# Kernel optimization log

Measured on AMD Instinct MI355X. Metric: run time of the kernel, lower is better.

Reference implementation:

```python
import jax, jax.numpy as jnp
import numpy as np
import math

V, B, C, H, W = 4, 8, 512, 16, 16
NH = 8


def setup_inputs() -> dict:
    key = jax.random.key(0)
    ks = jax.random.split(key, 10)
    def n(k, shape, s=1.0):
        return jax.random.normal(k, shape, dtype=jnp.float32) * s
    return dict(
        i=n(ks[0], (V, B, C, H, W)),
        c=n(ks[1], (V, B, C, H, W)),
        j=n(ks[2], (V, B, C, H, W)),
        ln1_g=jnp.ones((C,), jnp.float32), ln1_b=jnp.zeros((C,), jnp.float32),
        ln2_g=jnp.ones((C,), jnp.float32), ln2_b=jnp.zeros((C,), jnp.float32),
        Wq=n(ks[3], (C, C), 0.02), bq=jnp.zeros((C,), jnp.float32),
        Wkv=n(ks[4], (C, 2 * C), 0.02), bkv=jnp.zeros((2 * C,), jnp.float32),
        Wo=n(ks[5], (C, C), 0.02), bo=jnp.zeros((C,), jnp.float32),
        Wfc=n(ks[6], (C, 4 * C), 0.02), bfc=jnp.zeros((4 * C,), jnp.float32),
        Wpr=n(ks[7], (4 * C, C), 0.02), bpr=jnp.zeros((C,), jnp.float32),
    )


def _ln(x, g, b, eps=1e-5):
    mu = jnp.mean(x, axis=-1, keepdims=True)
    var = jnp.mean((x - mu) ** 2, axis=-1, keepdims=True)
    return (x - mu) * jax.lax.rsqrt(var + eps) * g + b


def _gelu_new(x):
    # 0.5*x*(1+tanh(sqrt(2/pi)*(x+0.044715*x^3)))
    k = math.sqrt(2.0 / math.pi)
    return 0.5 * x * (1.0 + jnp.tanh(k * (x + 0.044715 * x ** 3)))


def reference(i, c, j, ln1_g, ln1_b, ln2_g, ln2_b, Wq, bq, Wkv, bkv, Wo, bo, Wfc, bfc, Wpr, bpr):
    v, b, ch, h, w = i.shape
    T = v * h * w
    hd = ch // NH

    def to_seq(x):  # v b c h w -> b (v h w) c
        return jnp.transpose(x, (1, 0, 3, 4, 2)).reshape(b, T, ch)

    # LayerNorm (over channel dim) applied before attention
    qs = _ln(to_seq(i), ln1_g, ln1_b)   # [b, T, c]
    kvs = _ln(to_seq(j), ln1_g, ln1_b)  # [b, T, c]

    q = qs @ Wq + bq                    # [b, T, c]
    kv = kvs @ Wkv + bkv                # [b, T, 2c]
    k, vv = jnp.split(kv, 2, axis=-1)

    def heads(x):  # [b, T, c] -> [b, nh, T, hd]
        return x.reshape(b, T, NH, hd).transpose(0, 2, 1, 3)
    q, k, vv = heads(q), heads(k), heads(vv)

    # block-causal mask: token in view-block r attends to view-blocks <= r
    blk = jnp.arange(T) // (h * w)
    mask = blk[:, None] >= blk[None, :]  # [T, T] bool

    att = jnp.einsum('bhqd,bhkd->bhqk', q, k) * (1.0 / math.sqrt(hd))
    att = jnp.where(mask, att, -jnp.inf)
    att = jax.nn.softmax(att, axis=-1)
    y = jnp.einsum('bhqk,bhkd->bhqd', att, vv)
    y = y.transpose(0, 2, 1, 3).reshape(b, T, ch)
    y = y @ Wo + bo                     # attention output, seq layout

    # residual: ln1(c) + attn
    cs = _ln(to_seq(c), ln1_g, ln1_b) + y
    # MLP with residual
    hcs = _ln(cs, ln2_g, ln2_b)
    cs = cs + (_gelu_new(hcs @ Wfc + bfc) @ Wpr + bpr)

    # b (v h w) c -> v b c h w
    out = cs.reshape(b, v, h, w, ch).transpose(1, 0, 4, 2, 3)
    return out
```

## Files before the change

### kernel.cpp

```cpp
#include <hip/hip_runtime.h>
#include <hip/hip_bf16.h>
#include <math.h>


typedef __bf16 bf16;
typedef __bf16 bf16x8 __attribute__((ext_vector_type(8)));
typedef __bf16 bf16x4 __attribute__((ext_vector_type(4)));
typedef float  f32x4  __attribute__((ext_vector_type(4)));

__device__ __forceinline__ void gload_lds16(const void* g, void* l) {
  __builtin_amdgcn_global_load_lds(
      (__attribute__((address_space(1))) void*)(g),
      (__attribute__((address_space(3))) void*)(l), 16, 0, 0);
}

__global__ __launch_bounds__(256)
void prep_k(const float* __restrict__ Wq, const float* __restrict__ Wkv,
            const float* __restrict__ Wo, const float* __restrict__ Wfc,
            const float* __restrict__ Wpr,
            bf16* __restrict__ WqT, bf16* __restrict__ WkvT,
            bf16* __restrict__ WoT, bf16* __restrict__ WfcT,
            bf16* __restrict__ WprT,
            const float* __restrict__ xi, const float* __restrict__ xj,
            const float* __restrict__ xc,
            const float* __restrict__ g, const float* __restrict__ bb,
            bf16* __restrict__ qs, bf16* __restrict__ kvs,
            bf16* __restrict__ csb)
{
  __shared__ float tt[32][33];
  __shared__ float red[4][32];
  const int t = blockIdx.x;
  const int tid = threadIdx.x;
  if (t < 3072) {
    const float* W; bf16* Wt; int K, N, lognx, tl;
    if (t < 256)       { W = Wq;  Wt = WqT;  K = 512;  N = 512;  lognx = 4; tl = t; }
    else if (t < 768)  { W = Wkv; Wt = WkvT; K = 512;  N = 1024; lognx = 5; tl = t - 256; }
    else if (t < 1024) { W = Wo;  Wt = WoT;  K = 512;  N = 512;  lognx = 4; tl = t - 768; }
    else if (t < 2048) { W = Wfc; Wt = WfcT; K = 512;  N = 2048; lognx = 6; tl = t - 1024; }
    else               { W = Wpr; Wt = WprT; K = 2048; N = 512;  lognx = 4; tl = t - 2048; }
    const int bx = tl & ((1 << lognx) - 1), by = tl >> lognx;
    const int x = tid & 31, y = tid >> 5;
    const int n0 = bx << 5, k0 = by << 5;
#pragma unroll
    for (int yy = y; yy < 32; yy += 8)
      tt[yy][x] = W[(size_t)(k0 + yy) * N + n0 + x];
    __syncthreads();
#pragma unroll
    for (int yy = y; yy < 32; yy += 8)
      Wt[(size_t)(n0 + yy) * K + k0 + x] = (bf16)tt[x][yy];
    return;
  }
  const int u = t - 3072;
  const int sel = u >> 9, bid = u & 511;
  const int hh = bid & 15, b = (bid >> 4) & 7, v = bid >> 7;
  const float* src = (sel == 0) ? xi : ((sel == 1) ? xj : xc);
  const size_t base = ((size_t)(v * 8 + b) * 512) * 256 + (size_t)hh * 16;
  const int q = tid & 3, chb = tid >> 2;
  const int wid = tid >> 6, lane = tid & 63;
  const int cb = chb << 3;

  float gr[8], br[8];
  *(f32x4*)&gr[0] = *(const f32x4*)&g[cb];
  *(f32x4*)&gr[4] = *(const f32x4*)&g[cb + 4];
  *(f32x4*)&br[0] = *(const f32x4*)&bb[cb];
  *(f32x4*)&br[4] = *(const f32x4*)&bb[cb + 4];

  f32x4 x[8];
#pragma unroll
  for (int k = 0; k < 8; ++k)
    x[k] = *(const f32x4*)&src[base + (size_t)(cb + k) * 256 + (q << 2)];

  float s[4] = {0.f, 0.f, 0.f, 0.f}, ss[4] = {0.f, 0.f, 0.f, 0.f};
#pragma unroll
  for (int k = 0; k < 8; ++k)
#pragma unroll
    for (int i = 0; i < 4; ++i) {
      s[i] += x[k][i];
      ss[i] += x[k][i] * x[k][i];
    }
#pragma unroll
  for (int off = 4; off < 64; off <<= 1)
#pragma unroll
    for (int i = 0; i < 4; ++i) {
      s[i] += __shfl_xor(s[i], off);
      ss[i] += __shfl_xor(ss[i], off);
    }
  if (lane < 16) {
    red[wid][(lane & 3) * 4 + (lane >> 2)]      = s[lane >> 2];
    red[wid][16 + (lane & 3) * 4 + (lane >> 2)] = ss[lane >> 2];
  }
  __syncthreads();
  float mu[4], rs[4];
#pragma unroll
  for (int i = 0; i < 4; ++i) {
    const int e = q * 4 + i;
    float st  = red[0][e] + red[1][e] + red[2][e] + red[3][e];
    float sst = red[0][16 + e] + red[1][16 + e] + red[2][16 + e] + red[3][16 + e];
    mu[i] = st * (1.f / 512.f);
    rs[i] = rsqrtf(sst * (1.f / 512.f) - mu[i] * mu[i] + 1e-5f);
  }
  const int tkb = v * 256 + hh * 16 + (q << 2);
  bf16* dstb = (sel == 0) ? qs : ((sel == 1) ? kvs : csb);
#pragma unroll
  for (int i = 0; i < 4; ++i) {
    const size_t orow = ((size_t)b * 1024 + tkb + i) * 512;
    bf16x8 o;
#pragma unroll
    for (int k = 0; k < 8; ++k)
      o[k] = (bf16)((x[k][i] - mu[i]) * rs[i] * gr[k] + br[k]);
    *(bf16x8*)&dstb[orow + cb] = o;
  }
}

__global__ __launch_bounds__(256)
void ln2_k(const bf16* __restrict__ cs, const float* __restrict__ g,
           const float* __restrict__ bb, bf16* __restrict__ hcs)
{
  const int tid = threadIdx.x, wid = tid >> 6, lane = tid & 63;
  const int row = blockIdx.x * 4 + wid;
  const bf16x8 v8 = *(const bf16x8*)&cs[(size_t)row * 512 + lane * 8];
  float v[8];
#pragma unroll
  for (int k = 0; k < 8; ++k) v[k] = (float)v8[k];
  float s = 0.f, ss = 0.f;
#pragma unroll
  for (int k = 0; k < 8; ++k) { s += v[k]; ss += v[k] * v[k]; }
#pragma unroll
  for (int off = 1; off < 64; off <<= 1) {
    s += __shfl_xor(s, off);
    ss += __shfl_xor(ss, off);
  }
  const float mu = s * (1.f / 512.f);
  const float rstd = rsqrtf(ss * (1.f / 512.f) - mu * mu + 1e-5f);
  bf16x8 o;
#pragma unroll
  for (int k = 0; k < 8; ++k) {
    int ch = lane * 8 + k;
    o[k] = (bf16)((v[k] - mu) * rstd * g[ch] + bb[ch]);
  }
  *(bf16x8*)&hcs[(size_t)row * 512 + lane * 8] = o;
}

__global__ __launch_bounds__(256)
void gemm_fc_k(const bf16* __restrict__ A, const bf16* __restrict__ Bt,
               const float* __restrict__ bias, bf16* __restrict__ fo)
{
  const int K = 512;
  __shared__ __align__(16) char smem[34816];
  bf16* As = (bf16*)smem;
  bf16* Bs = (bf16*)(smem + 16384);
  const int tid = threadIdx.x;
  const int wid = tid >> 6, lane = tid & 63;
  const int wr = wid >> 1, wc = wid & 1;
  const int ml = lane & 15, kg = (lane >> 4) << 3;
  const int m0 = blockIdx.x * 128, n0 = blockIdx.y * 128;

  const int e0 = wid * 512 + lane * 8;
  const int r0 = e0 >> 5, c0 = e0 & 31;
  const int e1 = e0 + 2048;
  const int r1 = e1 >> 5, c1 = e1 & 31;

  const bf16* Ag = A + (size_t)m0 * K;
  const bf16* Bg = Bt + (size_t)n0 * K;

  f32x4 acc[4][4] = {};

  gload_lds16(Ag + (size_t)r0 * K + c0, As + wid * 512);
  gload_lds16(Ag + (size_t)r1 * K + c1, As + 2048 + wid * 512);
  gload_lds16(Bg + (size_t)r0 * K + c0, Bs + wid * 512);
  gload_lds16(Bg + (size_t)r1 * K + c1, Bs + 2048 + wid * 512);

  int cur = 0;
  for (int k0 = 0; k0 < K; k0 += 32) {
    __syncthreads();
    if (k0 + 32 < K) {
      const int nb = cur ^ 1, kn = k0 + 32;
      gload_lds16(Ag + (size_t)r0 * K + kn + c0, As + nb * 4096 + wid * 512);
      gload_lds16(Ag + (size_t)r1 * K + kn + c1, As + nb * 4096 + 2048 + wid * 512);
      gload_lds16(Bg + (size_t)r0 * K + kn + c0, Bs + nb * 4096 + wid * 512);
      gload_lds16(Bg + (size_t)r1 * K + kn + c1, Bs + nb * 4096 + 2048 + wid * 512);
    }
    bf16x8 af[4], bfr[4];
#pragma unroll
    for (int mf = 0; mf < 4; ++mf)
      af[mf] = *(const bf16x8*)&As[cur * 4096 + (wr * 64 + mf * 16 + ml) * 32 + kg];
#pragma unroll
    for (int nf = 0; nf < 4; ++nf)
      bfr[nf] = *(const bf16x8*)&Bs[cur * 4096 + (wc * 64 + nf * 16 + ml) * 32 + kg];
#pragma unroll
    for (int mf = 0; mf < 4; ++mf)
#pragma unroll
      for (int nf = 0; nf < 4; ++nf)
        acc[mf][nf] = __builtin_amdgcn_mfma_f32_16x16x32_bf16(
            af[mf], bfr[nf], acc[mf][nf], 0, 0, 0);
    cur ^= 1;
  }

  __syncthreads();
  bf16* OT = (bf16*)smem;
  const int jrow0 = (lane >> 4) << 2;
#pragma unroll
  for (int nf = 0; nf < 4; ++nf) {
    const float bv = bias[n0 + wc * 64 + nf * 16 + ml];
#pragma unroll
    for (int mf = 0; mf < 4; ++mf)
#pragma unroll
      for (int j = 0; j < 4; ++j) {
        float x = acc[mf][nf][j] + bv;
        float u = 0.7978845608f * (x + 0.044715f * x * x * x);
        float e = __expf(2.f * u);
        float th = 1.f - 2.f / (e + 1.f);
        OT[(wr * 64 + mf * 16 + jrow0 + j) * 132 + wc * 64 + nf * 16 + ml] =
            (bf16)(0.5f * x * (1.f + th));
      }
  }
  __syncthreads();
#pragma unroll
  for (int it = 0; it < 8; ++it) {
    const int idx = it * 256 + tid;
    const int cg = idx & 15, r = idx >> 4;
    *(bf16x8*)&fo[(size_t)(m0 + r) * 2048 + n0 + cg * 8] =
        *(const bf16x8*)&OT[r * 132 + cg * 8];
  }
}

enum { EPI_O = 2, EPI_PR = 4 };

template <int EPI>
__global__ __launch_bounds__(512)
void gemmsk_k(const bf16* __restrict__ A, const bf16* __restrict__ Bt,
              const float* __restrict__ bias, const bf16* res,
              void* out0, int K)
{
  __shared__ __align__(16) char smem[49152];
  bf16*  AS = (bf16*)smem;
  bf16*  BS = (bf16*)(smem + 16384);
  float* CF = (float*)smem;

  const int tid = threadIdx.x;
  const int wid = tid >> 6, lane = tid & 63;
  const int half = wid >> 2, w2 = wid & 3;
  const int wr = w2 >> 1, wc = w2 & 1;
  const int ml = lane & 15, kg = (lane >> 4) << 3;
  const int m0 = blockIdx.x * 64, n0 = blockIdx.y * 128;
  const int Kh = K >> 1;

  const int eA = w2 * 512 + lane * 8;
  const int rA = eA >> 5, cA = eA & 31;
  const int eB0 = (w2 * 2) * 512 + lane * 8;
  const int rB0 = eB0 >> 5, cB0 = eB0 & 31;
  const int eB1 = eB0 + 512;
  const int rB1 = eB1 >> 5, cB1 = eB1 & 31;

  const bf16* Ag = A + (size_t)m0 * K + half * Kh;
  const bf16* Bg = Bt + (size_t)n0 * K + half * Kh;

  f32x4 acc[2][4] = {};

  gload_lds16(Ag + (size_t)rA * K + cA, AS + half * 2048 + w2 * 512);
  gload_lds16(Bg + (size_t)rB0 * K + cB0, BS + half * 4096 + (w2 * 2) * 512);
  gload_lds16(Bg + (size_t)rB1 * K + cB1, BS + half * 4096 + (w2 * 2 + 1) * 512);

  int cur = 0;
  for (int k0 = 0; k0 < Kh; k0 += 32) {
    __syncthreads();
    if (k0 + 32 < Kh) {
      const int kn = k0 + 32, nb = cur ^ 1;
      gload_lds16(Ag + (size_t)rA * K + kn + cA,
                  AS + nb * 4096 + half * 2048 + w2 * 512);
      gload_lds16(Bg + (size_t)rB0 * K + kn + cB0,
                  BS + nb * 8192 + half * 4096 + (w2 * 2) * 512);
      gload_lds16(Bg + (size_t)rB1 * K + kn + cB1,
                  BS + nb * 8192 + half * 4096 + (w2 * 2 + 1) * 512);
    }
    const bf16* Ac = AS + cur * 4096 + half * 2048;
    const bf16* Bc = BS + cur * 8192 + half * 4096;
    bf16x8 af[2], bfr[4];
#pragma unroll
    for (int mf = 0; mf < 2; ++mf)
      af[mf] = *(const bf16x8*)&Ac[(wr * 32 + mf * 16 + ml) * 32 + kg];
#pragma unroll
    for (int nf = 0; nf < 4; ++nf)
      bfr[nf] = *(const bf16x8*)&Bc[(wc * 64 + nf * 16 + ml) * 32 + kg];
#pragma unroll
    for (int mf = 0; mf < 2; ++mf)
#pragma unroll
      for (int nf = 0; nf < 4; ++nf)
        acc[mf][nf] = __builtin_amdgcn_mfma_f32_16x16x32_bf16(
            af[mf], bfr[nf], acc[mf][nf], 0, 0, 0);
    cur ^= 1;
  }

  const int jrow0 = (lane >> 4) << 2;
  __syncthreads();
  if (half == 0) {
#pragma unroll
    for (int mf = 0; mf < 2; ++mf)
#pragma unroll
      for (int nf = 0; nf < 4; ++nf)
#pragma unroll
        for (int j = 0; j < 4; ++j)
          CF[(wr * 32 + mf * 16 + jrow0 + j) * 128 + wc * 64 + nf * 16 + ml] =
              acc[mf][nf][j];
  }
  __syncthreads();
  if (half == 1) {
#pragma unroll
    for (int nf = 0; nf < 4; ++nf) {
      const int n = n0 + wc * 64 + nf * 16 + ml;
      const float bv = bias[n];
#pragma unroll
      for (int mf = 0; mf < 2; ++mf) {
        const int mbase = m0 + wr * 32 + mf * 16 + jrow0;
        float v4[4];
#pragma unroll
        for (int j = 0; j < 4; ++j)
          v4[j] = acc[mf][nf][j] +
                  CF[(wr * 32 + mf * 16 + jrow0 + j) * 128 + wc * 64 + nf * 16 + ml];
        if constexpr (EPI == EPI_O) {
          bf16* cs = (bf16*)out0;
#pragma unroll
          for (int j = 0; j < 4; ++j) {
            const size_t idx = (size_t)(mbase + j) * 512 + n;
            cs[idx] = (bf16)(v4[j] + bv + (float)res[idx]);
          }
        } else {
          float* out = (float*)out0;
          const int b = mbase >> 10, t = mbase & 1023;
          const int v = t >> 8, hhh = (t >> 4) & 15, w0 = t & 15;
          f32x4 o;
#pragma unroll
          for (int j = 0; j < 4; ++j)
            o[j] = v4[j] + bv + (float)res[(size_t)(mbase + j) * 512 + n];
          *(f32x4*)&out[(((size_t)v * 8 + b) * 512 + n) * 256 + hhh * 16 + w0] = o;
        }
      }
    }
  }
}

__global__ __launch_bounds__(256)
void gemm_qkv_k(const bf16* __restrict__ Aq, const bf16* __restrict__ Akv,
                const bf16* __restrict__ WqT, const bf16* __restrict__ WkvT,
                const float* __restrict__ bq, const float* __restrict__ bkv,
                bf16* __restrict__ q_buf, bf16* __restrict__ k_buf,
                bf16* __restrict__ v_t)
{
  const int K = 512;
  __shared__ __align__(16) char smem[34816];
  bf16* As = (bf16*)smem;
  bf16* Bs = (bf16*)(smem + 16384);
  const int tid = threadIdx.x;
  const int wid = tid >> 6, lane = tid & 63;
  const int wr = wid >> 1, wc = wid & 1;
  const int ml = lane & 15, kg = (lane >> 4) << 3;
  const int ybl = blockIdx.y;
  const bool isq = ybl < 4;
  const bf16* A     = isq ? Aq  : Akv;
  const bf16* Bt    = isq ? WqT : WkvT;
  const float* bias = isq ? bq : bkv;
  const int n0 = isq ? (ybl << 7) : ((ybl - 4) << 7);
  const int m0 = blockIdx.x * 128;

  const int e0 = wid * 512 + lane * 8;
  const int r0 = e0 >> 5, c0 = e0 & 31;
  const int e1 = e0 + 2048;
  const int r1 = e1 >> 5, c1 = e1 & 31;

  const bf16* Ag = A + (size_t)m0 * K;
  const bf16* Bg = Bt + (size_t)n0 * K;

  f32x4 acc[4][4] = {};

  gload_lds16(Ag + (size_t)r0 * K + c0, As + wid * 512);
  gload_lds16(Ag + (size_t)r1 * K + c1, As + 2048 + wid * 512);
  gload_lds16(Bg + (size_t)r0 * K + c0, Bs + wid * 512);
  gload_lds16(Bg + (size_t)r1 * K + c1, Bs + 2048 + wid * 512);

  int cur = 0;
  for (int k0 = 0; k0 < K; k0 += 32) {
    __syncthreads();
    if (k0 + 32 < K) {
      const int nb = cur ^ 1, kn = k0 + 32;
      gload_lds16(Ag + (size_t)r0 * K + kn + c0, As + nb * 4096 + wid * 512);
      gload_lds16(Ag + (size_t)r1 * K + kn + c1, As + nb * 4096 + 2048 + wid * 512);
      gload_lds16(Bg + (size_t)r0 * K + kn + c0, Bs + nb * 4096 + wid * 512);
      gload_lds16(Bg + (size_t)r1 * K + kn + c1, Bs + nb * 4096 + 2048 + wid * 512);
    }
    bf16x8 af[4], bfr[4];
#pragma unroll
    for (int mf = 0; mf < 4; ++mf)
      af[mf] = *(const bf16x8*)&As[cur * 4096 + (wr * 64 + mf * 16 + ml) * 32 + kg];
#pragma unroll
    for (int nf = 0; nf < 4; ++nf)
      bfr[nf] = *(const bf16x8*)&Bs[cur * 4096 + (wc * 64 + nf * 16 + ml) * 32 + kg];
#pragma unroll
    for (int mf = 0; mf < 4; ++mf)
#pragma unroll
      for (int nf = 0; nf < 4; ++nf)
        acc[mf][nf] = __builtin_amdgcn_mfma_f32_16x16x32_bf16(
            af[mf], bfr[nf], acc[mf][nf], 0, 0, 0);
    cur ^= 1;
  }

  __syncthreads();
  bf16* OT = (bf16*)smem;
  const int jrow0 = (lane >> 4) << 2;
  const int b = m0 >> 10, t0 = m0 & 1023;
  if (ybl < 8) {
#pragma unroll
    for (int nf = 0; nf < 4; ++nf) {
      const float bv = bias[n0 + wc * 64 + nf * 16 + ml];
#pragma unroll
      for (int mf = 0; mf < 4; ++mf)
#pragma unroll
        for (int j = 0; j < 4; ++j)
          OT[(wr * 64 + mf * 16 + jrow0 + j) * 132 + wc * 64 + nf * 16 + ml] =
              (bf16)(acc[mf][nf][j] + bv);
    }
    __syncthreads();
    bf16* dst = isq ? q_buf : k_buf;
    const int h0 = n0 >> 6;
#pragma unroll
    for (int it = 0; it < 8; ++it) {
      const int idx = it * 256 + tid;
      const int dg = idx & 7, r = (idx >> 3) & 127, hl = idx >> 10;
      *(bf16x8*)&dst[(((size_t)b * 8 + h0 + hl) * 1024 + t0 + r) * 64 + dg * 8] =
          *(const bf16x8*)&OT[r * 132 + hl * 64 + dg * 8];
    }
  } else {
#pragma unroll
    for (int nf = 0; nf < 4; ++nf) {
      const float bv = bias[n0 + wc * 64 + nf * 16 + ml];
#pragma unroll
      for (int mf = 0; mf < 4; ++mf) {
        bf16x4 o;
#pragma unroll
        for (int j = 0; j < 4; ++j) o[j] = (bf16)(acc[mf][nf][j] + bv);
        *(bf16x4*)&OT[(wc * 64 + nf * 16 + ml) * 132 + wr * 64 + mf * 16 + jrow0] = o;
      }
    }
    __syncthreads();
    const int h0 = (n0 - 512) >> 6;
#pragma unroll
    for (int it = 0; it < 8; ++it) {
      const int idx = it * 256 + tid;
      const int og = idx & 15, c = idx >> 4;
      const int hl = c >> 6, d = c & 63;
      *(bf16x8*)&v_t[(((size_t)b * 8 + h0 + hl) * 64 + d) * 1024 + t0 + og * 8] =
          *(const bf16x8*)&OT[c * 132 + og * 8];
    }
  }
}

__global__ __launch_bounds__(256)
void attn_k(const bf16* __restrict__ qb, const bf16* __restrict__ kb,
            const bf16* __restrict__ vt, bf16* __restrict__ y)
{
  __shared__ bf16 Ks[2][4096];
  __shared__ bf16 Vs[2][4096];
  __shared__ bf16 Ps[4][1024];
  const int tid = threadIdx.x, wid = tid >> 6, lane = tid & 63;
  const int L = blockIdx.x;
  const int xcd = L & 7, chunk = L >> 3;
  const int bh = xcd + ((chunk >> 4) << 3);
  const int qt = 15 - (chunk & 15);
  const int b = bh >> 3, h = bh & 7;
  const int t0 = qt << 6;
  const int ml = lane & 15, hi = lane >> 4, kg = hi << 3;

  const bf16* qrow = qb + ((size_t)bh * 1024 + t0 + wid * 16) * 64;
  bf16x8 aq[2];
  aq[0] = *(const bf16x8*)&qrow[ml * 64 + kg];
  aq[1] = *(const bf16x8*)&qrow[ml * 64 + 32 + kg];

  f32x4 accO[4] = {};
  float lsum[4] = {0.f, 0.f, 0.f, 0.f};

  const int nkt = ((qt >> 2) + 1) << 2;
  const bf16* kbase = kb + (size_t)bh * 1024 * 64;
  const bf16* vbase = vt + (size_t)bh * 64 * 1024;

  const int sr = (wid << 3) + (lane >> 3);
  const int sg = ((lane & 7) ^ ((lane >> 3) & 7)) << 3;
  bf16* pw = &Ps[wid][0];

  {
    gload_lds16(kbase + (size_t)sr * 64 + sg,          &Ks[0][wid * 512]);
    gload_lds16(kbase + (size_t)(sr + 32) * 64 + sg,   &Ks[0][2048 + wid * 512]);
    gload_lds16(vbase + (size_t)sr * 1024 + sg,        &Vs[0][wid * 512]);
    gload_lds16(vbase + (size_t)(sr + 32) * 1024 + sg, &Vs[0][2048 + wid * 512]);
  }

  int cur = 0;
  for (int kt = 0; kt < nkt; ++kt) {
    __syncthreads();
    if (kt + 1 < nkt) {
      const int tk0 = (kt + 1) << 6;
      const int nb = cur ^ 1;
      gload_lds16(kbase + (size_t)(tk0 + sr) * 64 + sg,        &Ks[nb][wid * 512]);
      gload_lds16(kbase + (size_t)(tk0 + sr + 32) * 64 + sg,   &Ks[nb][2048 + wid * 512]);
      gload_lds16(vbase + (size_t)sr * 1024 + tk0 + sg,        &Vs[nb][wid * 512]);
      gload_lds16(vbase + (size_t)(sr + 32) * 1024 + tk0 + sg, &Vs[nb][2048 + wid * 512]);
    }

    f32x4 sa[4] = {};
    __builtin_amdgcn_s_setprio(1);
#pragma unroll
    for (int nf = 0; nf < 4; ++nf) {
      const int row = nf * 16 + ml;
#pragma unroll
      for (int ks = 0; ks < 2; ++ks) {
        const int g = ((ks * 4 + hi) ^ (ml & 7)) << 3;
        bf16x8 bk = *(const bf16x8*)&Ks[cur][row * 64 + g];
        sa[nf] = __builtin_amdgcn_mfma_f32_16x16x32_bf16(aq[ks], bk, sa[nf], 0, 0, 0);
      }
    }
    __builtin_amdgcn_s_setprio(0);

#pragma unroll
    for (int nf = 0; nf < 4; ++nf) {
      const int gp0 = nf * 2 + (ml >> 3);
#pragma unroll
      for (int j = 0; j < 4; ++j) {
        const float p = __expf(sa[nf][j] * 0.125f);
        lsum[j] += p;
        const int prow = (hi << 2) + j;
        pw[prow * 64 + ((gp0 ^ (prow & 7)) << 3) + (ml & 7)] = (bf16)p;
      }
    }

    __builtin_amdgcn_s_setprio(1);
#pragma unroll
    for (int ks = 0; ks < 2; ++ks) {
      const int g = ((ks * 4 + hi) ^ (ml & 7)) << 3;
      bf16x8 pa = *(const bf16x8*)&pw[ml * 64 + g];
#pragma unroll
      for (int df = 0; df < 4; ++df) {
        bf16x8 bv = *(const bf16x8*)&Vs[cur][(df * 16 + ml) * 64 + g];
        accO[df] = __builtin_amdgcn_mfma_f32_16x16x32_bf16(pa, bv, accO[df], 0, 0, 0);
      }
    }
    __builtin_amdgcn_s_setprio(0);
    cur ^= 1;
  }

  float inv[4];
#pragma unroll
  for (int j = 0; j < 4; ++j) {
    float s = lsum[j];
#pragma unroll
    for (int off = 1; off < 16; off <<= 1) s += __shfl_xor(s, off);
    inv[j] = 1.f / s;
  }
#pragma unroll
  for (int df = 0; df < 4; ++df)
#pragma unroll
    for (int j = 0; j < 4; ++j) {
      const int t = t0 + wid * 16 + (hi << 2) + j;
      const int c = h * 64 + df * 16 + ml;
      y[((size_t)b * 1024 + t) * 512 + c] = (bf16)(accO[df][j] * inv[j]);
    }
}

extern "C" void kernel_launch(void* const* d_in, const int* in_sizes, int n_in,
                              void* d_out, int out_size, void* d_ws, size_t ws_size,
                              hipStream_t stream)
{
  const float* xi    = (const float*)d_in[0];
  const float* xc    = (const float*)d_in[1];
  const float* xj    = (const float*)d_in[2];
  const float* ln1_g = (const float*)d_in[3];
  const float* ln1_b = (const float*)d_in[4];
  const float* ln2_g = (const float*)d_in[5];
  const float* ln2_b = (const float*)d_in[6];
  const float* Wq    = (const float*)d_in[7];
  const float* bq    = (const float*)d_in[8];
  const float* Wkv   = (const float*)d_in[9];
  const float* bkv   = (const float*)d_in[10];
  const float* Wo    = (const float*)d_in[11];
  const float* bo    = (const float*)d_in[12];
  const float* Wfc   = (const float*)d_in[13];
  const float* bfc   = (const float*)d_in[14];
  const float* Wpr   = (const float*)d_in[15];
  const float* bpr   = (const float*)d_in[16];

  char* ws = (char*)d_ws;
  const size_t MB = 1ull << 20;
  bf16*  qs    = (bf16*)(ws + 0);
  bf16*  kvs   = (bf16*)(ws + 8 * MB);
  bf16*  csb   = (bf16*)(ws + 16 * MB);
  bf16*  WqT   = (bf16*)(ws + 32 * MB);
  bf16*  WkvT  = (bf16*)(ws + 32 * MB + 512 * 1024);
  bf16*  WoT   = (bf16*)(ws + 33 * MB + 512 * 1024);
  bf16*  WfcT  = (bf16*)(ws + 34 * MB);
  bf16*  WprT  = (bf16*)(ws + 36 * MB);
  bf16*  q_buf = (bf16*)(ws + 38 * MB);
  bf16*  k_buf = (bf16*)(ws + 46 * MB);
  bf16*  v_t   = (bf16*)(ws + 54 * MB);
  bf16*  yb    = (bf16*)(ws + 0);
  bf16*  hcs   = (bf16*)(ws + 8 * MB);
  bf16*  fcact = (bf16*)(ws + 38 * MB);

  prep_k<<<dim3(4608), 256, 0, stream>>>(Wq, Wkv, Wo, Wfc, Wpr,
                                         WqT, WkvT, WoT, WfcT, WprT,
                                         xi, xj, xc, ln1_g, ln1_b, qs, kvs, csb);

  gemm_qkv_k<<<dim3(64, 12), 256, 0, stream>>>(qs, kvs, WqT, WkvT, bq, bkv,
                                               q_buf, k_buf, v_t);

  attn_k<<<dim3(1024), 256, 0, stream>>>(q_buf, k_buf, v_t, yb);

  gemmsk_k<EPI_O><<<dim3(128, 4), 512, 0, stream>>>(yb, WoT, bo, csb,
                                                    (void*)csb, 512);

  ln2_k<<<dim3(2048), 256, 0, stream>>>(csb, ln2_g, ln2_b, hcs);

  gemm_fc_k<<<dim3(64, 16), 256, 0, stream>>>(hcs, WfcT, bfc, fcact);

  gemmsk_k<EPI_PR><<<dim3(128, 4), 512, 0, stream>>>(fcact, WprT, bpr, csb,
                                                     d_out, 2048);

  (void)in_sizes; (void)n_in; (void)out_size; (void)ws_size;
}
```

Baseline: 169.9 us.

## Split prep kernel into wider-vectorized weight transpose and LayerNorm kernels

The combined weight-transpose and LN1 prep kernel is split into two launches. The transpose now uses 64x64 tiles with float4 global loads and 16-byte bf16x8 stores, where it previously did scalar 32x32 element moves. The LayerNorm part has each block cover 32 tokens and each thread 16 channels, giving wider bf16 stores and an f32x4 cross-wave reduction. This is meant to cut per-element memory transactions and block counts, at the cost of one extra kernel launch.

Measured after the change: 162.6 us. -4.3%, faster.

```diff
diff --git a/kernel.cpp b/kernel.cpp
--- a/kernel.cpp
+++ b/kernel.cpp
@@ -15,100 +15,119 @@
 }
 
 __global__ __launch_bounds__(256)
-void prep_k(const float* __restrict__ Wq, const float* __restrict__ Wkv,
-            const float* __restrict__ Wo, const float* __restrict__ Wfc,
-            const float* __restrict__ Wpr,
-            bf16* __restrict__ WqT, bf16* __restrict__ WkvT,
-            bf16* __restrict__ WoT, bf16* __restrict__ WfcT,
-            bf16* __restrict__ WprT,
-            const float* __restrict__ xi, const float* __restrict__ xj,
-            const float* __restrict__ xc,
-            const float* __restrict__ g, const float* __restrict__ bb,
-            bf16* __restrict__ qs, bf16* __restrict__ kvs,
-            bf16* __restrict__ csb)
-{
-  __shared__ float tt[32][33];
-  __shared__ float red[4][32];
+void prep_w_k(const float* __restrict__ Wq, const float* __restrict__ Wkv,
+              const float* __restrict__ Wo, const float* __restrict__ Wfc,
+              const float* __restrict__ Wpr,
+              bf16* __restrict__ WqT, bf16* __restrict__ WkvT,
+              bf16* __restrict__ WoT, bf16* __restrict__ WfcT,
+              bf16* __restrict__ WprT)
+{
+  __shared__ float tile[64 * 65];
   const int t = blockIdx.x;
   const int tid = threadIdx.x;
-  if (t < 3072) {
-    const float* W; bf16* Wt; int K, N, lognx, tl;
-    if (t < 256)       { W = Wq;  Wt = WqT;  K = 512;  N = 512;  lognx = 4; tl = t; }
-    else if (t < 768)  { W = Wkv; Wt = WkvT; K = 512;  N = 1024; lognx = 5; tl = t - 256; }
-    else if (t < 1024) { W = Wo;  Wt = WoT;  K = 512;  N = 512;  lognx = 4; tl = t - 768; }
-    else if (t < 2048) { W = Wfc; Wt = WfcT; K = 512;  N = 2048; lognx = 6; tl = t - 1024; }
-    else               { W = Wpr; Wt = WprT; K = 2048; N = 512;  lognx = 4; tl = t - 2048; }
-    const int bx = tl & ((1 << lognx) - 1), by = tl >> lognx;
-    const int x = tid & 31, y = tid >> 5;
-    const int n0 = bx << 5, k0 = by << 5;
-#pragma unroll
-    for (int yy = y; yy < 32; yy += 8)
-      tt[yy][x] = W[(size_t)(k0 + yy) * N + n0 + x];
-    __syncthreads();
-#pragma unroll
-    for (int yy = y; yy < 32; yy += 8)
-      Wt[(size_t)(n0 + yy) * K + k0 + x] = (bf16)tt[x][yy];
-    return;
-  }
-  const int u = t - 3072;
-  const int sel = u >> 9, bid = u & 511;
-  const int hh = bid & 15, b = (bid >> 4) & 7, v = bid >> 7;
+  const float* W; bf16* Wt; int K, N, nx, tl;
+  if (t < 64)        { W = Wq;  Wt = WqT;  K = 512;  N = 512;  nx = 8;  tl = t; }
+  else if (t < 192)  { W = Wkv; Wt = WkvT; K = 512;  N = 1024; nx = 16; tl = t - 64; }
+  else if (t < 256)  { W = Wo;  Wt = WoT;  K = 512;  N = 512;  nx = 8;  tl = t - 192; }
+  else if (t < 512)  { W = Wfc; Wt = WfcT; K = 512;  N = 2048; nx = 32; tl = t - 256; }
+  else               { W = Wpr; Wt = WprT; K = 2048; N = 512;  nx = 8;  tl = t - 512; }
+  const int bx = tl % nx, by = tl / nx;
+  const int n0 = bx << 6, k0 = by << 6;
+
+  const int xl = tid & 15, yl = tid >> 4;
+#pragma unroll
+  for (int r = 0; r < 4; ++r) {
+    const int row = yl + r * 16;
+    const f32x4 vv = *(const f32x4*)&W[(size_t)(k0 + row) * N + n0 + xl * 4];
+#pragma unroll
+    for (int e = 0; e < 4; ++e)
+      tile[row * 65 + xl * 4 + e] = vv[e];
+  }
+  __syncthreads();
+  const int xk = tid & 7, nl = tid >> 3;
+#pragma unroll
+  for (int r2 = 0; r2 < 2; ++r2) {
+    const int n = nl + r2 * 32;
+    bf16x8 o;
+#pragma unroll
+    for (int e = 0; e < 8; ++e)
+      o[e] = (bf16)tile[(xk * 8 + e) * 65 + n];
+    *(bf16x8*)&Wt[(size_t)(n0 + n) * K + k0 + xk * 8] = o;
+  }
+}
+
+__global__ __launch_bounds__(256)
+void prep_ln_k(const float* __restrict__ xi, const float* __restrict__ xj,
+               const float* __restrict__ xc,
+               const float* __restrict__ g, const float* __restrict__ bb,
+               bf16* __restrict__ qs, bf16* __restrict__ kvs,
+               bf16* __restrict__ csb)
+{
+  __shared__ __align__(16) float red[4][64];
+  const int tid = threadIdx.x;
+  const int u = blockIdx.x;
+  const int sel = u >> 8, bid = u & 255;
+  const int hp = bid & 7, b = (bid >> 3) & 7, v = bid >> 6;
   const float* src = (sel == 0) ? xi : ((sel == 1) ? xj : xc);
-  const size_t base = ((size_t)(v * 8 + b) * 512) * 256 + (size_t)hh * 16;
-  const int q = tid & 3, chb = tid >> 2;
-  const int wid = tid >> 6, lane = tid & 63;
-  const int cb = chb << 3;
-
-  float gr[8], br[8];
-  *(f32x4*)&gr[0] = *(const f32x4*)&g[cb];
-  *(f32x4*)&gr[4] = *(const f32x4*)&g[cb + 4];
-  *(f32x4*)&br[0] = *(const f32x4*)&bb[cb];
-  *(f32x4*)&br[4] = *(const f32x4*)&bb[cb + 4];
-
-  f32x4 x[8];
-#pragma unroll
-  for (int k = 0; k < 8; ++k)
-    x[k] = *(const f32x4*)&src[base + (size_t)(cb + k) * 256 + (q << 2)];
+  const size_t base = ((size_t)(v * 8 + b) * 512) * 256 + hp * 32;
+  const int q8 = tid & 7, chb = tid >> 3;
+  const int wid = tid >> 6, lc = (tid >> 3) & 7;
+  const int cb = chb << 4;
+
+  float gr[16], br[16];
+#pragma unroll
+  for (int p = 0; p < 4; ++p) {
+    *(f32x4*)&gr[p * 4] = *(const f32x4*)&g[cb + p * 4];
+    *(f32x4*)&br[p * 4] = *(const f32x4*)&bb[cb + p * 4];
+  }
+  f32x4 x[16];
+#pragma unroll
+  for (int k = 0; k < 16; ++k)
+    x[k] = *(const f32x4*)&src[base + (size_t)(cb + k) * 256 + q8 * 4];
 
   float s[4] = {0.f, 0.f, 0.f, 0.f}, ss[4] = {0.f, 0.f, 0.f, 0.f};
 #pragma unroll
-  for (int k = 0; k < 8; ++k)
+  for (int k = 0; k < 16; ++k)
 #pragma unroll
     for (int i = 0; i < 4; ++i) {
       s[i] += x[k][i];
       ss[i] += x[k][i] * x[k][i];
     }
 #pragma unroll
-  for (int off = 4; off < 64; off <<= 1)
+  for (int off = 8; off < 64; off <<= 1)
 #pragma unroll
     for (int i = 0; i < 4; ++i) {
       s[i] += __shfl_xor(s[i], off);
       ss[i] += __shfl_xor(ss[i], off);
     }
-  if (lane < 16) {
-    red[wid][(lane & 3) * 4 + (lane >> 2)]      = s[lane >> 2];
-    red[wid][16 + (lane & 3) * 4 + (lane >> 2)] = ss[lane >> 2];
-  }
+  if (lc < 4)      red[wid][q8 * 4 + lc]      = s[lc];
+  else             red[wid][32 + q8 * 4 + (lc - 4)] = ss[lc - 4];
   __syncthreads();
+  f32x4 st = {0.f, 0.f, 0.f, 0.f}, sst = {0.f, 0.f, 0.f, 0.f};
+#pragma unroll
+  for (int w = 0; w < 4; ++w) {
+    st  += *(const f32x4*)&red[w][q8 * 4];
+    sst += *(const f32x4*)&red[w][32 + q8 * 4];
+  }
   float mu[4], rs[4];
 #pragma unroll
   for (int i = 0; i < 4; ++i) {
-    const int e = q * 4 + i;
-    float st  = red[0][e] + red[1][e] + red[2][e] + red[3][e];
-    float sst = red[0][16 + e] + red[1][16 + e] + red[2][16 + e] + red[3][16 + e];
-    mu[i] = st * (1.f / 512.f);
-    rs[i] = rsqrtf(sst * (1.f / 512.f) - mu[i] * mu[i] + 1e-5f);
-  }
-  const int tkb = v * 256 + hh * 16 + (q << 2);
+    mu[i] = st[i] * (1.f / 512.f);
+    rs[i] = rsqrtf(sst[i] * (1.f / 512.f) - mu[i] * mu[i] + 1e-5f);
+  }
   bf16* dstb = (sel == 0) ? qs : ((sel == 1) ? kvs : csb);
+  const int tkb = v * 256 + hp * 32 + q8 * 4;
 #pragma unroll
   for (int i = 0; i < 4; ++i) {
-    const size_t orow = ((size_t)b * 1024 + tkb + i) * 512;
-    bf16x8 o;
-#pragma unroll
-    for (int k = 0; k < 8; ++k)
-      o[k] = (bf16)((x[k][i] - mu[i]) * rs[i] * gr[k] + br[k]);
-    *(bf16x8*)&dstb[orow + cb] = o;
+    const size_t orow = ((size_t)b * 1024 + tkb + i) * 512 + cb;
+    bf16x8 o0, o1;
+#pragma unroll
+    for (int k = 0; k < 8; ++k) {
+      o0[k] = (bf16)((x[k][i] - mu[i]) * rs[i] * gr[k] + br[k]);
+      o1[k] = (bf16)((x[k + 8][i] - mu[i]) * rs[i] * gr[k + 8] + br[k + 8]);
+    }
+    *(bf16x8*)&dstb[orow]     = o0;
+    *(bf16x8*)&dstb[orow + 8] = o1;
   }
 }
 
@@ -602,9 +621,10 @@
   bf16*  hcs   = (bf16*)(ws + 8 * MB);
   bf16*  fcact = (bf16*)(ws + 38 * MB);
 
-  prep_k<<<dim3(4608), 256, 0, stream>>>(Wq, Wkv, Wo, Wfc, Wpr,
-                                         WqT, WkvT, WoT, WfcT, WprT,
-                                         xi, xj, xc, ln1_g, ln1_b, qs, kvs, csb);
+  prep_w_k<<<dim3(768), 256, 0, stream>>>(Wq, Wkv, Wo, Wfc, Wpr,
+                                          WqT, WkvT, WoT, WfcT, WprT);
+  prep_ln_k<<<dim3(768), 256, 0, stream>>>(xi, xj, xc, ln1_g, ln1_b,
+                                           qs, kvs, csb);
 
   gemm_qkv_k<<<dim3(64, 12), 256, 0, stream>>>(qs, kvs, WqT, WkvT, bq, bkv,
                                                q_buf, k_buf, v_t);
```
